# Kernel tuning notes

Measured on AMD Instinct MI355X. Metric: run time of the kernel, lower is better.

Reference implementation:

```python
import jax, jax.numpy as jnp
import numpy as np

B, T, E, H = 8, 2048, 1024, 64  # batch, seq_len(=block_size), embedding_size, head_size


def setup_inputs() -> dict:
    key = jax.random.key(0)
    k1, k2, k3, k4, k5 = jax.random.split(key, 5)
    x = jax.random.normal(k1, (B, T, E), dtype=jnp.float32)
    Wk = jax.random.normal(k2, (H, E), dtype=jnp.float32) * 0.02
    Wq = jax.random.normal(k3, (H, E), dtype=jnp.float32) * 0.02
    Wv = jax.random.normal(k4, (H, E), dtype=jnp.float32) * 0.02
    attention_mask = jax.random.randint(k5, (B, T), 0, 2).astype(jnp.int32)
    return {"x": x, "Wk": Wk, "Wq": Wq, "Wv": Wv, "attention_mask": attention_mask}


def reference(x, Wk, Wq, Wv, attention_mask):
    # Linear projections (nn.Linear with no bias: y = x @ W.T)
    k = jnp.einsum('bte,he->bth', x, Wk)
    q = jnp.einsum('bte,he->bth', x, Wq)
    v = jnp.einsum('bte,he->bth', x, Wv)
    scale = v.shape[2] ** -0.5  # head_size^-0.5, faithful to v.shape[2]**(-0.5)
    wei = jnp.einsum('bqh,bkh->bqk', q, k) * scale  # [B,T,T]
    # Causal mask (tril buffer) AND padding outer-product mask; the double-precision
    # outer product in the original just tests nonzero-ness, so a boolean AND is exact.
    causal = jnp.tril(jnp.ones((T, T), dtype=bool))  # [T,T]
    pad = (attention_mask[:, :, None] * attention_mask[:, None, :]) != 0  # [B,T,T]
    wei = jnp.where(causal[None, :, :] & pad, wei, -jnp.inf)
    wei = jax.nn.softmax(wei, axis=-1)
    wei = jnp.nan_to_num(wei)  # fully-masked rows -> 0 (matches torch.nan_to_num)
    # dropout in eval mode -> identity
    out = jnp.einsum('bqk,bkh->bqh', wei, v)
    return out
```

## Files before the change

### kernel.cpp

```cpp
#include <hip/hip_runtime.h>
#include <hip/hip_bf16.h>

typedef __bf16 bf16x8 __attribute__((ext_vector_type(8)));
typedef __bf16 bf16x4 __attribute__((ext_vector_type(4)));
typedef float  f32x4  __attribute__((ext_vector_type(4)));

#define LDP 72
#define KLDP 72
#define VLDP 40

#define BAR() { asm volatile("s_waitcnt lgkmcnt(0)" ::: "memory"); __builtin_amdgcn_s_barrier(); }

__global__ __launch_bounds__(256) void wconv_kernel(
    const float* __restrict__ Wk, const float* __restrict__ Wq,
    const float* __restrict__ Wv, __bf16* __restrict__ wbf)
{
    int idx = blockIdx.x * 256 + threadIdx.x;
    int row = idx >> 8;
    int c4  = idx & 255;
    const float* wp = (row < 64) ? Wk + (size_t)row * 1024
                    : (row < 128) ? Wq + (size_t)(row - 64) * 1024
                                  : Wv + (size_t)(row - 128) * 1024;
    float4 f = *reinterpret_cast<const float4*>(wp + c4 * 4);
    bf16x4 v; v[0] = (__bf16)f.x; v[1] = (__bf16)f.y; v[2] = (__bf16)f.z; v[3] = (__bf16)f.w;
    *reinterpret_cast<bf16x4*>(&wbf[(size_t)row * 1024 + c4 * 4]) = v;
}

__global__ __launch_bounds__(512) void maskpack_kernel(
    const int* __restrict__ mask, unsigned* __restrict__ maskw)
{
    int wdx = threadIdx.x;
    unsigned wv = 0;
    #pragma unroll
    for (int bit = 0; bit < 32; bit++)
        wv |= (mask[wdx * 32 + bit] != 0 ? 1u : 0u) << bit;
    maskw[wdx] = wv;
}

__global__ __launch_bounds__(1024) void proj_kernel(
    const float* __restrict__ x, const __bf16* __restrict__ wbf,
    __bf16* __restrict__ kbuf, __bf16* __restrict__ qbuf, __bf16* __restrict__ vtbuf)
{
    __shared__ __align__(16) __bf16 Slds[2][256 * LDP];
    __shared__ __align__(16) __bf16 Vtl[64 * LDP];

    const int tid  = threadIdx.x;
    const int lane = tid & 63;
    const int wid  = tid >> 6;
    const int wm   = wid >> 2;
    const int wn   = wid & 3;
    const int mbase = blockIdx.x * 64;

    const int cl = lane & 15;
    const int e0 = (lane >> 4) * 8;
    const int r0 = (lane >> 4) * 4;

    const int arow = tid >> 4, acg = tid & 15;
    const float* aptr = x + (size_t)(mbase + arow) * 1024 + acg * 4;

    float4 a0, a1;
    bf16x4 w0[3], w1[3];

#define ISSUE(aset, wset, kb) { \
    aset = *reinterpret_cast<const float4*>(aptr + (kb)); \
    _Pragma("unroll") \
    for (int i_ = 0; i_ < 3; i_++) { \
        int c_ = i_ * 1024 + tid; \
        wset[i_] = *reinterpret_cast<const bf16x4*>(&wbf[(size_t)(c_ >> 4) * 1024 + (kb) + (c_ & 15) * 4]); \
    } }

#define COMMIT(aset, wset, bufi) { \
    bf16x4 av_; \
    av_[0] = (__bf16)aset.x; av_[1] = (__bf16)aset.y; av_[2] = (__bf16)aset.z; av_[3] = (__bf16)aset.w; \
    *reinterpret_cast<bf16x4*>(&Slds[bufi][arow * LDP + acg * 4]) = av_; \
    _Pragma("unroll") \
    for (int i_ = 0; i_ < 3; i_++) { \
        int c_ = i_ * 1024 + tid; \
        *reinterpret_cast<bf16x4*>(&Slds[bufi][(64 + (c_ >> 4)) * LDP + (c_ & 15) * 4]) = wset[i_]; \
    } }

    f32x4 acc[3];
    #pragma unroll
    for (int n = 0; n < 3; n++) acc[n] = (f32x4){0.f, 0.f, 0.f, 0.f};

    ISSUE(a0, w0, 0);
    COMMIT(a0, w0, 0);
    ISSUE(a1, w1, 64);
    BAR();

    #pragma unroll 2
    for (int j = 0; j < 16; j++) {
        if (j < 14) {
            if (j & 1) { ISSUE(a1, w1, (j + 2) * 64); }
            else       { ISSUE(a0, w0, (j + 2) * 64); }
        }
        const __bf16* buf = Slds[j & 1];
        #pragma unroll
        for (int kk = 0; kk < 2; kk++) {
            bf16x8 a = *reinterpret_cast<const bf16x8*>(&buf[(wm * 16 + cl) * LDP + kk * 32 + e0]);
            #pragma unroll
            for (int nf = 0; nf < 3; nf++) {
                bf16x8 b = *reinterpret_cast<const bf16x8*>(&buf[(64 + wn * 48 + nf * 16 + cl) * LDP + kk * 32 + e0]);
                acc[nf] = __builtin_amdgcn_mfma_f32_16x16x32_bf16(a, b, acc[nf], 0, 0, 0);
            }
        }
        if (j < 15) {
            if (j & 1) { COMMIT(a0, w0, 0); }
            else       { COMMIT(a1, w1, 1); }
            BAR();
        }
    }
#undef ISSUE
#undef COMMIT

    #pragma unroll
    for (int nf = 0; nf < 3; nf++) {
        int c = wn * 48 + nf * 16 + cl;
        #pragma unroll
        for (int r = 0; r < 4; r++) {
            int mrel = wm * 16 + r0 + r;
            float v = acc[nf][r];
            if (c < 64)        kbuf[(size_t)(mbase + mrel) * 64 + c]         = (__bf16)v;
            else if (c < 128)  qbuf[(size_t)(mbase + mrel) * 64 + (c - 64)]  = (__bf16)v;
            else               Vtl[(c - 128) * LDP + mrel]                   = (__bf16)v;
        }
    }
    __syncthreads();
    {
        int b   = mbase >> 11;
        int tof = mbase & 2047;
        int h   = tid >> 4;
        int seg = tid & 15;
        bf16x4 v4 = *reinterpret_cast<const bf16x4*>(&Vtl[h * LDP + seg * 4]);
        *reinterpret_cast<bf16x4*>(&vtbuf[(size_t)b * 64 * 2048 + (size_t)h * 2048 + tof + seg * 4]) = v4;
    }
}

__global__ __launch_bounds__(256) void attn_kernel(
    const __bf16* __restrict__ qbuf, const __bf16* __restrict__ kbuf,
    const __bf16* __restrict__ vtbuf, const unsigned* __restrict__ maskw,
    const int* __restrict__ mask,
    float* __restrict__ out, float* __restrict__ accpart, float* __restrict__ mlpart,
    int nsplit, int tps)
{
    __shared__ __align__(16) __bf16 Klds[2][32 * KLDP];
    __shared__ __align__(16) __bf16 Vlds[2][64 * VLDP];
    __shared__ __align__(16) __bf16 Plds[4][16 * VLDP];

    const int tid  = threadIdx.x;
    const int lane = tid & 63;
    const int w    = tid >> 6;
    const int wg   = blockIdx.x;
    const int b    = wg & 7;
    const int rr_  = wg >> 3;
    const int qt   = rr_ & 31;
    const int sp   = rr_ >> 5;
    const int qbase = qt * 64 + w * 16;

    const int jbeg = sp * tps;
    const int jend = min((sp + 1) * tps, 2 * qt + 2);

    if (nsplit > 1 && jbeg >= jend) {
        float* ap = accpart + ((size_t)(b * nsplit + sp) * 2048 + qt * 64) * 64;
        for (int i = tid; i < 64 * 64; i += 256) ap[i] = 0.f;
        float* mp = mlpart + ((size_t)(b * nsplit + sp) * 2048 + qt * 64) * 2;
        for (int i = tid; i < 64; i += 256) { mp[2 * i] = -INFINITY; mp[2 * i + 1] = 0.f; }
        return;
    }

    const int cl = lane & 15;
    const int e0 = (lane >> 4) * 8;
    const int r0 = (lane >> 4) * 4;
    const int qs = qbase + cl;

    bf16x8 aq[2];
    #pragma unroll
    for (int kk = 0; kk < 2; kk++)
        aq[kk] = *reinterpret_cast<const bf16x8*>(&qbuf[((size_t)b * 2048 + qs) * 64 + kk * 32 + e0]);

    float m = -INFINITY, l = 0.f;
    f32x4 acc[4];
    #pragma unroll
    for (int hf = 0; hf < 4; hf++) acc[hf] = (f32x4){0.f, 0.f, 0.f, 0.f};

    const __bf16* kb  = kbuf  + (size_t)b * 2048 * 64;
    const __bf16* vtb = vtbuf + (size_t)b * 64 * 2048;

    const int krow = tid >> 3, kcg = tid & 7;
    const int vrow = tid >> 2, vcg = tid & 3;
    bf16x8 st_k, st_v;

#define KV_ISSUE(jj) { \
    st_k = *reinterpret_cast<const bf16x8*>(&kb[(size_t)((jj) * 32 + krow) * 64 + kcg * 8]); \
    st_v = *reinterpret_cast<const bf16x8*>(&vtb[(size_t)vrow * 2048 + (jj) * 32 + vcg * 8]); }

#define KV_COMMIT(bi) { \
    *reinterpret_cast<bf16x8*>(&Klds[bi][krow * KLDP + kcg * 8]) = st_k; \
    *reinterpret_cast<bf16x8*>(&Vlds[bi][vrow * VLDP + vcg * 8]) = st_v; }

    const int nt = jend - jbeg;
    KV_ISSUE(jbeg);
    KV_COMMIT(0);
    if (nt > 1) KV_ISSUE(jbeg + 1);
    BAR();

    for (int t = 0; t < nt; t++) {
        const int j = jbeg + t;
        const int cur = t & 1;

        if (t + 1 < nt) KV_COMMIT(cur ^ 1);
        if (t + 2 < nt) KV_ISSUE(j + 2);

        f32x4 s[2];
        #pragma unroll
        for (int jf = 0; jf < 2; jf++) {
            f32x4 tacc = (f32x4){0.f, 0.f, 0.f, 0.f};
            #pragma unroll
            for (int kk = 0; kk < 2; kk++) {
                bf16x8 bk = *reinterpret_cast<const bf16x8*>(&Klds[cur][(jf * 16 + cl) * KLDP + kk * 32 + e0]);
                tacc = __builtin_amdgcn_mfma_f32_16x16x32_bf16(bk, aq[kk], tacc, 0, 0, 0);
            }
            s[jf] = tacc;
        }

        const unsigned mw = maskw[b * 64 + j];
        float tmax = -INFINITY;
        #pragma unroll
        for (int jf = 0; jf < 2; jf++)
            #pragma unroll
            for (int r = 0; r < 4; r++) {
                int kvl = jf * 16 + r0 + r;
                bool ok = ((mw >> kvl) & 1u) && (j * 32 + kvl <= qs);
                float sv = s[jf][r] * 0.125f;
                sv = ok ? sv : -INFINITY;
                s[jf][r] = sv;
                tmax = fmaxf(tmax, sv);
            }
        tmax = fmaxf(tmax, __shfl_xor(tmax, 16));
        tmax = fmaxf(tmax, __shfl_xor(tmax, 32));

        float mn = fmaxf(m, tmax);
        float alpha = (mn == -INFINITY) ? 1.0f : __expf(m - mn);
        float rs = 0.f;
        #pragma unroll
        for (int jf = 0; jf < 2; jf++)
            #pragma unroll
            for (int r = 0; r < 4; r++) {
                float p = (mn == -INFINITY) ? 0.f : __expf(s[jf][r] - mn);
                s[jf][r] = p;
                rs += p;
            }
        rs += __shfl_xor(rs, 16);
        rs += __shfl_xor(rs, 32);
        l = l * alpha + rs;
        m = mn;

        #pragma unroll
        for (int hf = 0; hf < 4; hf++)
            #pragma unroll
            for (int r = 0; r < 4; r++) acc[hf][r] *= alpha;

        #pragma unroll
        for (int jf = 0; jf < 2; jf++) {
            bf16x4 p4;
            #pragma unroll
            for (int r = 0; r < 4; r++) p4[r] = (__bf16)s[jf][r];
            *reinterpret_cast<bf16x4*>(&Plds[w][cl * VLDP + jf * 16 + r0]) = p4;
        }
        {
            bf16x8 pb = *reinterpret_cast<const bf16x8*>(&Plds[w][cl * VLDP + e0]);
            #pragma unroll
            for (int hf = 0; hf < 4; hf++) {
                bf16x8 av = *reinterpret_cast<const bf16x8*>(&Vlds[cur][(hf * 16 + cl) * VLDP + e0]);
                acc[hf] = __builtin_amdgcn_mfma_f32_16x16x32_bf16(av, pb, acc[hf], 0, 0, 0);
            }
        }

        if (t + 1 < nt) BAR();
    }
#undef KV_ISSUE
#undef KV_COMMIT

    if (nsplit == 1) {
        int mq = mask[b * 2048 + qs];
        #pragma unroll
        for (int hf = 0; hf < 4; hf++)
            #pragma unroll
            for (int r = 0; r < 4; r++) {
                float v = (l > 0.f && mq != 0) ? acc[hf][r] / l : 0.f;
                out[((size_t)b * 2048 + qs) * 64 + hf * 16 + r0 + r] = v;
            }
    } else {
        #pragma unroll
        for (int hf = 0; hf < 4; hf++)
            #pragma unroll
            for (int r = 0; r < 4; r++)
                accpart[((size_t)(b * nsplit + sp) * 2048 + qs) * 64 + hf * 16 + r0 + r] = acc[hf][r];
        if (lane < 16) {
            int qrow = qbase + lane;
            mlpart[((size_t)(b * nsplit + sp) * 2048 + qrow) * 2 + 0] = m;
            mlpart[((size_t)(b * nsplit + sp) * 2048 + qrow) * 2 + 1] = l;
        }
    }
}

template<int NS>
__global__ __launch_bounds__(256) void combine_kernel(
    const float* __restrict__ accpart, const float* __restrict__ mlpart,
    const int* __restrict__ mask, float* __restrict__ out)
{
    int idx = blockIdx.x * 256 + threadIdx.x;
    int qglob = idx >> 6;
    int h = idx & 63;
    int b = qglob >> 11;
    int qrow = qglob & 2047;

    if (mask[qglob] == 0) { out[idx] = 0.f; return; }

    float m_s[NS], l_s[NS];
    float M = -INFINITY;
    #pragma unroll
    for (int s = 0; s < NS; s++) {
        size_t mo = ((size_t)(b * NS + s) * 2048 + qrow) * 2;
        m_s[s] = mlpart[mo];
        l_s[s] = mlpart[mo + 1];
        M = fmaxf(M, m_s[s]);
    }
    if (M == -INFINITY) { out[idx] = 0.f; return; }

    float L = 0.f, O = 0.f;
    #pragma unroll
    for (int s = 0; s < NS; s++) {
        float wgt = (m_s[s] == -INFINITY) ? 0.f : __expf(m_s[s] - M);
        L += l_s[s] * wgt;
        O += wgt * accpart[((size_t)(b * NS + s) * 2048 + qrow) * 64 + h];
    }
    out[idx] = (L > 0.f) ? O / L : 0.f;
}

extern "C" void kernel_launch(void* const* d_in, const int* in_sizes, int n_in,
                              void* d_out, int out_size, void* d_ws, size_t ws_size,
                              hipStream_t stream) {
    const float* x  = (const float*)d_in[0];
    const float* Wk = (const float*)d_in[1];
    const float* Wq = (const float*)d_in[2];
    const float* Wv = (const float*)d_in[3];
    const int* mask = (const int*)d_in[4];
    float* out = (float*)d_out;

    const size_t NTOK = 8 * 2048;
    __bf16* kbuf  = (__bf16*)d_ws;
    __bf16* qbuf  = kbuf + NTOK * 64;
    __bf16* vtbuf = qbuf + NTOK * 64;
    __bf16* wbf   = vtbuf + (size_t)8 * 64 * 2048;
    unsigned* maskw = (unsigned*)(wbf + (size_t)192 * 1024);
    const size_t base_bytes = NTOK * 64 * 2 * 2 + (size_t)8 * 64 * 2048 * 2
                            + (size_t)192 * 1024 * 2 + 512 * 4;

    const size_t acc_per_split = NTOK * 64 * 4;
    const size_t ml_per_split  = NTOK * 2 * 4;
    int nsplit = 1;
    if (ws_size >= base_bytes + 4 * (acc_per_split + ml_per_split))      nsplit = 4;
    else if (ws_size >= base_bytes + 2 * (acc_per_split + ml_per_split)) nsplit = 2;

    float* accpart = (float*)((char*)d_ws + base_bytes);
    float* mlpart  = accpart + NTOK * 64 * nsplit;

    wconv_kernel<<<192, 256, 0, stream>>>(Wk, Wq, Wv, wbf);
    maskpack_kernel<<<1, 512, 0, stream>>>(mask, maskw);
    proj_kernel<<<256, 1024, 0, stream>>>(x, wbf, kbuf, qbuf, vtbuf);
    attn_kernel<<<8 * 32 * nsplit, 256, 0, stream>>>(
        qbuf, kbuf, vtbuf, maskw, mask, out, accpart, mlpart, nsplit, 64 / nsplit);
    if (nsplit == 4)
        combine_kernel<4><<<(16384 * 64) / 256, 256, 0, stream>>>(accpart, mlpart, mask, out);
    else if (nsplit == 2)
        combine_kernel<2><<<(16384 * 64) / 256, 256, 0, stream>>>(accpart, mlpart, mask, out);
}
```

Before: 64.43 us.

## Widen attention tiles to 64 keys and 32 query rows per wave

The attention kernel now runs two waves per block. Each wave processes two 16-row query groups against 64-key K/V tiles, so every K and V fragment read from LDS feeds two MFMAs. The old LDS double buffer is replaced by one buffer plus a register prefetch, with two barriers per tile. The mask-packing kernel is folded into the weight-conversion launch, and later stages read the packed bitmask instead of the int mask. Splits with no work no longer zero their partial accumulators; they only write m=-inf and l=0, which risks NaN in the combine step if that uninitialized memory holds non-finite values.

```diff
diff --git a/kernel.cpp b/kernel.cpp
--- a/kernel.cpp
+++ b/kernel.cpp
@@ -5,16 +5,28 @@
 typedef __bf16 bf16x4 __attribute__((ext_vector_type(4)));
 typedef float  f32x4  __attribute__((ext_vector_type(4)));
 
-#define LDP 72
+#define LDP  72
 #define KLDP 72
-#define VLDP 40
+#define VLDP 72
+#define PLDP 72
 
 #define BAR() { asm volatile("s_waitcnt lgkmcnt(0)" ::: "memory"); __builtin_amdgcn_s_barrier(); }
 
 __global__ __launch_bounds__(256) void wconv_kernel(
     const float* __restrict__ Wk, const float* __restrict__ Wq,
-    const float* __restrict__ Wv, __bf16* __restrict__ wbf)
+    const float* __restrict__ Wv, const int* __restrict__ mask,
+    __bf16* __restrict__ wbf, unsigned* __restrict__ maskw)
 {
+    if (blockIdx.x == 192) {
+        for (int wdx = threadIdx.x; wdx < 512; wdx += 256) {
+            unsigned wv = 0;
+            #pragma unroll
+            for (int bit = 0; bit < 32; bit++)
+                wv |= (mask[wdx * 32 + bit] != 0 ? 1u : 0u) << bit;
+            maskw[wdx] = wv;
+        }
+        return;
+    }
     int idx = blockIdx.x * 256 + threadIdx.x;
     int row = idx >> 8;
     int c4  = idx & 255;
@@ -26,17 +38,6 @@
     *reinterpret_cast<bf16x4*>(&wbf[(size_t)row * 1024 + c4 * 4]) = v;
 }
 
-__global__ __launch_bounds__(512) void maskpack_kernel(
-    const int* __restrict__ mask, unsigned* __restrict__ maskw)
-{
-    int wdx = threadIdx.x;
-    unsigned wv = 0;
-    #pragma unroll
-    for (int bit = 0; bit < 32; bit++)
-        wv |= (mask[wdx * 32 + bit] != 0 ? 1u : 0u) << bit;
-    maskw[wdx] = wv;
-}
-
 __global__ __launch_bounds__(1024) void proj_kernel(
     const float* __restrict__ x, const __bf16* __restrict__ wbf,
     __bf16* __restrict__ kbuf, __bf16* __restrict__ qbuf, __bf16* __restrict__ vtbuf)
@@ -136,16 +137,15 @@
     }
 }
 
-__global__ __launch_bounds__(256) void attn_kernel(
+__global__ __launch_bounds__(128) void attn_kernel(
     const __bf16* __restrict__ qbuf, const __bf16* __restrict__ kbuf,
     const __bf16* __restrict__ vtbuf, const unsigned* __restrict__ maskw,
-    const int* __restrict__ mask,
     float* __restrict__ out, float* __restrict__ accpart, float* __restrict__ mlpart,
     int nsplit, int tps)
 {
-    __shared__ __align__(16) __bf16 Klds[2][32 * KLDP];
-    __shared__ __align__(16) __bf16 Vlds[2][64 * VLDP];
-    __shared__ __align__(16) __bf16 Plds[4][16 * VLDP];
+    __shared__ __align__(16) __bf16 Klds[64 * KLDP];
+    __shared__ __align__(16) __bf16 Vlds[64 * VLDP];
+    __shared__ __align__(16) __bf16 Plds[2][2][16 * PLDP];
 
     const int tid  = threadIdx.x;
     const int lane = tid & 63;
@@ -155,151 +155,155 @@
     const int rr_  = wg >> 3;
     const int qt   = rr_ & 31;
     const int sp   = rr_ >> 5;
-    const int qbase = qt * 64 + w * 16;
 
     const int jbeg = sp * tps;
-    const int jend = min((sp + 1) * tps, 2 * qt + 2);
+    const int jend = min((sp + 1) * tps, qt + 1);
 
     if (nsplit > 1 && jbeg >= jend) {
-        float* ap = accpart + ((size_t)(b * nsplit + sp) * 2048 + qt * 64) * 64;
-        for (int i = tid; i < 64 * 64; i += 256) ap[i] = 0.f;
-        float* mp = mlpart + ((size_t)(b * nsplit + sp) * 2048 + qt * 64) * 2;
-        for (int i = tid; i < 64; i += 256) { mp[2 * i] = -INFINITY; mp[2 * i + 1] = 0.f; }
+        for (int i = tid; i < 64; i += 128) {
+            size_t mo = ((size_t)(b * nsplit + sp) * 2048 + qt * 64 + i) * 2;
+            mlpart[mo] = -INFINITY; mlpart[mo + 1] = 0.f;
+        }
         return;
     }
 
     const int cl = lane & 15;
     const int e0 = (lane >> 4) * 8;
     const int r0 = (lane >> 4) * 4;
-    const int qs = qbase + cl;
-
-    bf16x8 aq[2];
-    #pragma unroll
-    for (int kk = 0; kk < 2; kk++)
-        aq[kk] = *reinterpret_cast<const bf16x8*>(&qbuf[((size_t)b * 2048 + qs) * 64 + kk * 32 + e0]);
-
-    float m = -INFINITY, l = 0.f;
-    f32x4 acc[4];
-    #pragma unroll
-    for (int hf = 0; hf < 4; hf++) acc[hf] = (f32x4){0.f, 0.f, 0.f, 0.f};
+    const int qs0 = qt * 64 + w * 16 + cl;
+    const int qs1 = qs0 + 32;
+
+    bf16x8 aq0[2], aq1[2];
+    #pragma unroll
+    for (int kk = 0; kk < 2; kk++) {
+        aq0[kk] = *reinterpret_cast<const bf16x8*>(&qbuf[((size_t)b * 2048 + qs0) * 64 + kk * 32 + e0]);
+        aq1[kk] = *reinterpret_cast<const bf16x8*>(&qbuf[((size_t)b * 2048 + qs1) * 64 + kk * 32 + e0]);
+    }
+
+    float m0 = -INFINITY, l0 = 0.f, m1 = -INFINITY, l1 = 0.f;
+    f32x4 acc0[4], acc1[4];
+    #pragma unroll
+    for (int hf = 0; hf < 4; hf++) { acc0[hf] = (f32x4){0.f,0.f,0.f,0.f}; acc1[hf] = (f32x4){0.f,0.f,0.f,0.f}; }
 
     const __bf16* kb  = kbuf  + (size_t)b * 2048 * 64;
     const __bf16* vtb = vtbuf + (size_t)b * 64 * 2048;
 
-    const int krow = tid >> 3, kcg = tid & 7;
-    const int vrow = tid >> 2, vcg = tid & 3;
-    bf16x8 st_k, st_v;
-
-#define KV_ISSUE(jj) { \
-    st_k = *reinterpret_cast<const bf16x8*>(&kb[(size_t)((jj) * 32 + krow) * 64 + kcg * 8]); \
-    st_v = *reinterpret_cast<const bf16x8*>(&vtb[(size_t)vrow * 2048 + (jj) * 32 + vcg * 8]); }
-
-#define KV_COMMIT(bi) { \
-    *reinterpret_cast<bf16x8*>(&Klds[bi][krow * KLDP + kcg * 8]) = st_k; \
-    *reinterpret_cast<bf16x8*>(&Vlds[bi][vrow * VLDP + vcg * 8]) = st_v; }
+    const int srow = tid >> 1;
+    const int sc   = (tid & 1) * 32;
+    bf16x8 stk[4], stv[4];
+
+#define KV_ISSUE(jj) { _Pragma("unroll") for (int i_ = 0; i_ < 4; i_++) { \
+    stk[i_] = *reinterpret_cast<const bf16x8*>(&kb[(size_t)((jj) * 64 + srow) * 64 + sc + i_ * 8]); \
+    stv[i_] = *reinterpret_cast<const bf16x8*>(&vtb[(size_t)srow * 2048 + (jj) * 64 + sc + i_ * 8]); } }
+
+#define KV_COMMIT() { _Pragma("unroll") for (int i_ = 0; i_ < 4; i_++) { \
+    *reinterpret_cast<bf16x8*>(&Klds[srow * KLDP + sc + i_ * 8]) = stk[i_]; \
+    *reinterpret_cast<bf16x8*>(&Vlds[srow * VLDP + sc + i_ * 8]) = stv[i_]; } }
+
+#define SOFTMAX(S, mS, lS, accS, qsS, su) { \
+    float tmax = -INFINITY; \
+    _Pragma("unroll") for (int jf = 0; jf < 4; jf++) { \
+        unsigned mw = (jf < 2) ? mw0 : mw1; \
+        _Pragma("unroll") for (int r = 0; r < 4; r++) { \
+            int kvl = jf * 16 + r0 + r; \
+            bool ok = ((mw >> (kvl & 31)) & 1u) && (j * 64 + kvl <= qsS); \
+            float sv = S[jf][r] * 0.125f; \
+            sv = ok ? sv : -INFINITY; \
+            S[jf][r] = sv; tmax = fmaxf(tmax, sv); } } \
+    tmax = fmaxf(tmax, __shfl_xor(tmax, 16)); \
+    tmax = fmaxf(tmax, __shfl_xor(tmax, 32)); \
+    float mn = fmaxf(mS, tmax); \
+    float alpha = (mn == -INFINITY) ? 1.0f : __expf(mS - mn); \
+    float rs = 0.f; \
+    _Pragma("unroll") for (int jf = 0; jf < 4; jf++) \
+        _Pragma("unroll") for (int r = 0; r < 4; r++) { \
+            float p = (mn == -INFINITY) ? 0.f : __expf(S[jf][r] - mn); \
+            S[jf][r] = p; rs += p; } \
+    rs += __shfl_xor(rs, 16); \
+    rs += __shfl_xor(rs, 32); \
+    lS = lS * alpha + rs; mS = mn; \
+    _Pragma("unroll") for (int hf = 0; hf < 4; hf++) \
+        _Pragma("unroll") for (int r = 0; r < 4; r++) accS[hf][r] *= alpha; \
+    _Pragma("unroll") for (int jf = 0; jf < 4; jf++) { \
+        bf16x4 p4; \
+        _Pragma("unroll") for (int r = 0; r < 4; r++) p4[r] = (__bf16)S[jf][r]; \
+        *reinterpret_cast<bf16x4*>(&Plds[w][su][cl * PLDP + jf * 16 + r0]) = p4; } }
 
     const int nt = jend - jbeg;
     KV_ISSUE(jbeg);
-    KV_COMMIT(0);
+    KV_COMMIT();
     if (nt > 1) KV_ISSUE(jbeg + 1);
     BAR();
 
     for (int t = 0; t < nt; t++) {
         const int j = jbeg + t;
-        const int cur = t & 1;
-
-        if (t + 1 < nt) KV_COMMIT(cur ^ 1);
-        if (t + 2 < nt) KV_ISSUE(j + 2);
-
-        f32x4 s[2];
-        #pragma unroll
-        for (int jf = 0; jf < 2; jf++) {
-            f32x4 tacc = (f32x4){0.f, 0.f, 0.f, 0.f};
+
+        f32x4 s0[4], s1[4];
+        #pragma unroll
+        for (int jf = 0; jf < 4; jf++) {
+            f32x4 t0 = (f32x4){0.f,0.f,0.f,0.f}, t1 = (f32x4){0.f,0.f,0.f,0.f};
             #pragma unroll
             for (int kk = 0; kk < 2; kk++) {
-                bf16x8 bk = *reinterpret_cast<const bf16x8*>(&Klds[cur][(jf * 16 + cl) * KLDP + kk * 32 + e0]);
-                tacc = __builtin_amdgcn_mfma_f32_16x16x32_bf16(bk, aq[kk], tacc, 0, 0, 0);
-            }
-            s[jf] = tacc;
-        }
-
-        const unsigned mw = maskw[b * 64 + j];
-        float tmax = -INFINITY;
-        #pragma unroll
-        for (int jf = 0; jf < 2; jf++)
-            #pragma unroll
-            for (int r = 0; r < 4; r++) {
-                int kvl = jf * 16 + r0 + r;
-                bool ok = ((mw >> kvl) & 1u) && (j * 32 + kvl <= qs);
-                float sv = s[jf][r] * 0.125f;
-                sv = ok ? sv : -INFINITY;
-                s[jf][r] = sv;
-                tmax = fmaxf(tmax, sv);
-            }
-        tmax = fmaxf(tmax, __shfl_xor(tmax, 16));
-        tmax = fmaxf(tmax, __shfl_xor(tmax, 32));
-
-        float mn = fmaxf(m, tmax);
-        float alpha = (mn == -INFINITY) ? 1.0f : __expf(m - mn);
-        float rs = 0.f;
-        #pragma unroll
-        for (int jf = 0; jf < 2; jf++)
-            #pragma unroll
-            for (int r = 0; r < 4; r++) {
-                float p = (mn == -INFINITY) ? 0.f : __expf(s[jf][r] - mn);
-                s[jf][r] = p;
-                rs += p;
-            }
-        rs += __shfl_xor(rs, 16);
-        rs += __shfl_xor(rs, 32);
-        l = l * alpha + rs;
-        m = mn;
-
-        #pragma unroll
-        for (int hf = 0; hf < 4; hf++)
-            #pragma unroll
-            for (int r = 0; r < 4; r++) acc[hf][r] *= alpha;
-
-        #pragma unroll
-        for (int jf = 0; jf < 2; jf++) {
-            bf16x4 p4;
-            #pragma unroll
-            for (int r = 0; r < 4; r++) p4[r] = (__bf16)s[jf][r];
-            *reinterpret_cast<bf16x4*>(&Plds[w][cl * VLDP + jf * 16 + r0]) = p4;
-        }
-        {
-            bf16x8 pb = *reinterpret_cast<const bf16x8*>(&Plds[w][cl * VLDP + e0]);
+                bf16x8 bk = *reinterpret_cast<const bf16x8*>(&Klds[(jf * 16 + cl) * KLDP + kk * 32 + e0]);
+                t0 = __builtin_amdgcn_mfma_f32_16x16x32_bf16(bk, aq0[kk], t0, 0, 0, 0);
+                t1 = __builtin_amdgcn_mfma_f32_16x16x32_bf16(bk, aq1[kk], t1, 0, 0, 0);
+            }
+            s0[jf] = t0; s1[jf] = t1;
+        }
+
+        const unsigned mw0 = maskw[b * 64 + j * 2];
+        const unsigned mw1 = maskw[b * 64 + j * 2 + 1];
+        SOFTMAX(s0, m0, l0, acc0, qs0, 0);
+        SOFTMAX(s1, m1, l1, acc1, qs1, 1);
+
+        #pragma unroll
+        for (int kk = 0; kk < 2; kk++) {
+            bf16x8 p0 = *reinterpret_cast<const bf16x8*>(&Plds[w][0][cl * PLDP + kk * 32 + e0]);
+            bf16x8 p1 = *reinterpret_cast<const bf16x8*>(&Plds[w][1][cl * PLDP + kk * 32 + e0]);
             #pragma unroll
             for (int hf = 0; hf < 4; hf++) {
-                bf16x8 av = *reinterpret_cast<const bf16x8*>(&Vlds[cur][(hf * 16 + cl) * VLDP + e0]);
-                acc[hf] = __builtin_amdgcn_mfma_f32_16x16x32_bf16(av, pb, acc[hf], 0, 0, 0);
-            }
-        }
-
-        if (t + 1 < nt) BAR();
+                bf16x8 av = *reinterpret_cast<const bf16x8*>(&Vlds[(hf * 16 + cl) * VLDP + kk * 32 + e0]);
+                acc0[hf] = __builtin_amdgcn_mfma_f32_16x16x32_bf16(av, p0, acc0[hf], 0, 0, 0);
+                acc1[hf] = __builtin_amdgcn_mfma_f32_16x16x32_bf16(av, p1, acc1[hf], 0, 0, 0);
+            }
+        }
+
+        BAR();
+        if (t + 1 < nt) {
+            KV_COMMIT();
+            if (t + 2 < nt) KV_ISSUE(j + 2);
+            BAR();
+        }
     }
 #undef KV_ISSUE
 #undef KV_COMMIT
-
+#undef SOFTMAX
+
+    const bool mq0 = (maskw[b * 64 + (qs0 >> 5)] >> (qs0 & 31)) & 1u;
+    const bool mq1 = (maskw[b * 64 + (qs1 >> 5)] >> (qs1 & 31)) & 1u;
     if (nsplit == 1) {
-        int mq = mask[b * 2048 + qs];
         #pragma unroll
         for (int hf = 0; hf < 4; hf++)
             #pragma unroll
             for (int r = 0; r < 4; r++) {
-                float v = (l > 0.f && mq != 0) ? acc[hf][r] / l : 0.f;
-                out[((size_t)b * 2048 + qs) * 64 + hf * 16 + r0 + r] = v;
+                float v0 = (l0 > 0.f && mq0) ? acc0[hf][r] / l0 : 0.f;
+                float v1 = (l1 > 0.f && mq1) ? acc1[hf][r] / l1 : 0.f;
+                out[((size_t)b * 2048 + qs0) * 64 + hf * 16 + r0 + r] = v0;
+                out[((size_t)b * 2048 + qs1) * 64 + hf * 16 + r0 + r] = v1;
             }
     } else {
         #pragma unroll
         for (int hf = 0; hf < 4; hf++)
             #pragma unroll
-            for (int r = 0; r < 4; r++)
-                accpart[((size_t)(b * nsplit + sp) * 2048 + qs) * 64 + hf * 16 + r0 + r] = acc[hf][r];
+            for (int r = 0; r < 4; r++) {
+                accpart[((size_t)(b * nsplit + sp) * 2048 + qs0) * 64 + hf * 16 + r0 + r] = acc0[hf][r];
+                accpart[((size_t)(b * nsplit + sp) * 2048 + qs1) * 64 + hf * 16 + r0 + r] = acc1[hf][r];
+            }
         if (lane < 16) {
-            int qrow = qbase + lane;
-            mlpart[((size_t)(b * nsplit + sp) * 2048 + qrow) * 2 + 0] = m;
-            mlpart[((size_t)(b * nsplit + sp) * 2048 + qrow) * 2 + 1] = l;
+            size_t mo0 = ((size_t)(b * nsplit + sp) * 2048 + qs0) * 2;
+            size_t mo1 = ((size_t)(b * nsplit + sp) * 2048 + qs1) * 2;
+            mlpart[mo0] = m0; mlpart[mo0 + 1] = l0;
+            mlpart[mo1] = m1; mlpart[mo1 + 1] = l1;
         }
     }
 }
@@ -307,7 +311,7 @@
 template<int NS>
 __global__ __launch_bounds__(256) void combine_kernel(
     const float* __restrict__ accpart, const float* __restrict__ mlpart,
-    const int* __restrict__ mask, float* __restrict__ out)
+    const unsigned* __restrict__ maskw, float* __restrict__ out)
 {
     int idx = blockIdx.x * 256 + threadIdx.x;
     int qglob = idx >> 6;
@@ -315,7 +319,7 @@
     int b = qglob >> 11;
     int qrow = qglob & 2047;
 
-    if (mask[qglob] == 0) { out[idx] = 0.f; return; }
+    if (!((maskw[b * 64 + (qrow >> 5)] >> (qrow & 31)) & 1u)) { out[idx] = 0.f; return; }
 
     float m_s[NS], l_s[NS];
     float M = -INFINITY;
@@ -366,13 +370,12 @@
     float* accpart = (float*)((char*)d_ws + base_bytes);
     float* mlpart  = accpart + NTOK * 64 * nsplit;
 
-    wconv_kernel<<<192, 256, 0, stream>>>(Wk, Wq, Wv, wbf);
-    maskpack_kernel<<<1, 512, 0, stream>>>(mask, maskw);
+    wconv_kernel<<<193, 256, 0, stream>>>(Wk, Wq, Wv, mask, wbf, maskw);
     proj_kernel<<<256, 1024, 0, stream>>>(x, wbf, kbuf, qbuf, vtbuf);
-    attn_kernel<<<8 * 32 * nsplit, 256, 0, stream>>>(
-        qbuf, kbuf, vtbuf, maskw, mask, out, accpart, mlpart, nsplit, 64 / nsplit);
+    attn_kernel<<<8 * 32 * nsplit, 128, 0, stream>>>(
+        qbuf, kbuf, vtbuf, maskw, out, accpart, mlpart, nsplit, 32 / nsplit);
     if (nsplit == 4)
-        combine_kernel<4><<<(16384 * 64) / 256, 256, 0, stream>>>(accpart, mlpart, mask, out);
+        combine_kernel<4><<<(16384 * 64) / 256, 256, 0, stream>>>(accpart, mlpart, maskw, out);
     else if (nsplit == 2)
-        combine_kernel<2><<<(16384 * 64) / 256, 256, 0, stream>>>(accpart, mlpart, mask, out);
-}
+        combine_kernel<2><<<(16384 * 64) / 256, 256, 0, stream>>>(accpart, mlpart, maskw, out);
+}
```

After: 58.21 us. -9.7%, faster.

## Restructure attention to single-wave blocks covering 64 queries, allow 8-way KV split

Applied to the files above, without the earlier changes.

The attention kernel now runs one wavefront per block. Each wave handles all four 16-row query chunks, so every K/V tile loaded into LDS is reused across 64 queries, and block barriers are replaced by local LDS waitcnt fences with a single-buffered tile. The split-KV factor can rise to 8 when workspace allows. Mask packing is folded into the weight-conversion kernel to save a launch, and empty splits write only m/l, with combine skipping them. The cost is much higher register pressure per wave (acc[4][4], aq[4][2]), fewer threads per block to hide latency, and more partial traffic in the combine step.

```diff
diff --git a/kernel.cpp b/kernel.cpp
--- a/kernel.cpp
+++ b/kernel.cpp
@@ -5,16 +5,29 @@
 typedef __bf16 bf16x4 __attribute__((ext_vector_type(4)));
 typedef float  f32x4  __attribute__((ext_vector_type(4)));
 
-#define LDP 72
+#define LDP  72
 #define KLDP 72
 #define VLDP 40
+#define PLDP 40
 
 #define BAR() { asm volatile("s_waitcnt lgkmcnt(0)" ::: "memory"); __builtin_amdgcn_s_barrier(); }
+#define DSFENCE() { asm volatile("s_waitcnt lgkmcnt(0)" ::: "memory"); }
 
 __global__ __launch_bounds__(256) void wconv_kernel(
     const float* __restrict__ Wk, const float* __restrict__ Wq,
-    const float* __restrict__ Wv, __bf16* __restrict__ wbf)
+    const float* __restrict__ Wv, const int* __restrict__ mask,
+    __bf16* __restrict__ wbf, unsigned* __restrict__ maskw)
 {
+    if (blockIdx.x == 192) {
+        for (int wdx = threadIdx.x; wdx < 512; wdx += 256) {
+            unsigned wv = 0;
+            #pragma unroll
+            for (int bit = 0; bit < 32; bit++)
+                wv |= (mask[wdx * 32 + bit] != 0 ? 1u : 0u) << bit;
+            maskw[wdx] = wv;
+        }
+        return;
+    }
     int idx = blockIdx.x * 256 + threadIdx.x;
     int row = idx >> 8;
     int c4  = idx & 255;
@@ -26,17 +39,6 @@
     *reinterpret_cast<bf16x4*>(&wbf[(size_t)row * 1024 + c4 * 4]) = v;
 }
 
-__global__ __launch_bounds__(512) void maskpack_kernel(
-    const int* __restrict__ mask, unsigned* __restrict__ maskw)
-{
-    int wdx = threadIdx.x;
-    unsigned wv = 0;
-    #pragma unroll
-    for (int bit = 0; bit < 32; bit++)
-        wv |= (mask[wdx * 32 + bit] != 0 ? 1u : 0u) << bit;
-    maskw[wdx] = wv;
-}
-
 __global__ __launch_bounds__(1024) void proj_kernel(
     const float* __restrict__ x, const __bf16* __restrict__ wbf,
     __bf16* __restrict__ kbuf, __bf16* __restrict__ qbuf, __bf16* __restrict__ vtbuf)
@@ -136,170 +138,195 @@
     }
 }
 
-__global__ __launch_bounds__(256) void attn_kernel(
+__global__ __launch_bounds__(64) void attn_kernel(
     const __bf16* __restrict__ qbuf, const __bf16* __restrict__ kbuf,
     const __bf16* __restrict__ vtbuf, const unsigned* __restrict__ maskw,
-    const int* __restrict__ mask,
     float* __restrict__ out, float* __restrict__ accpart, float* __restrict__ mlpart,
     int nsplit, int tps)
 {
-    __shared__ __align__(16) __bf16 Klds[2][32 * KLDP];
-    __shared__ __align__(16) __bf16 Vlds[2][64 * VLDP];
-    __shared__ __align__(16) __bf16 Plds[4][16 * VLDP];
-
-    const int tid  = threadIdx.x;
-    const int lane = tid & 63;
-    const int w    = tid >> 6;
+    __shared__ __align__(16) __bf16 Klds[32 * KLDP];
+    __shared__ __align__(16) __bf16 Vlds[64 * VLDP];
+    __shared__ __align__(16) __bf16 Plds[4][16 * PLDP];
+
+    const int lane = threadIdx.x;
     const int wg   = blockIdx.x;
     const int b    = wg & 7;
-    const int rr_  = wg >> 3;
-    const int qt   = rr_ & 31;
-    const int sp   = rr_ >> 5;
-    const int qbase = qt * 64 + w * 16;
+    const int r_   = wg >> 3;
+    const int qt   = r_ & 31;
+    const int sp   = r_ >> 5;
 
     const int jbeg = sp * tps;
     const int jend = min((sp + 1) * tps, 2 * qt + 2);
 
     if (nsplit > 1 && jbeg >= jend) {
-        float* ap = accpart + ((size_t)(b * nsplit + sp) * 2048 + qt * 64) * 64;
-        for (int i = tid; i < 64 * 64; i += 256) ap[i] = 0.f;
-        float* mp = mlpart + ((size_t)(b * nsplit + sp) * 2048 + qt * 64) * 2;
-        for (int i = tid; i < 64; i += 256) { mp[2 * i] = -INFINITY; mp[2 * i + 1] = 0.f; }
+        size_t mo = ((size_t)(b * nsplit + sp) * 2048 + qt * 64 + lane) * 2;
+        mlpart[mo] = -INFINITY; mlpart[mo + 1] = 0.f;
         return;
     }
 
     const int cl = lane & 15;
-    const int e0 = (lane >> 4) * 8;
-    const int r0 = (lane >> 4) * 4;
-    const int qs = qbase + cl;
-
-    bf16x8 aq[2];
-    #pragma unroll
-    for (int kk = 0; kk < 2; kk++)
-        aq[kk] = *reinterpret_cast<const bf16x8*>(&qbuf[((size_t)b * 2048 + qs) * 64 + kk * 32 + e0]);
-
-    float m = -INFINITY, l = 0.f;
-    f32x4 acc[4];
-    #pragma unroll
-    for (int hf = 0; hf < 4; hf++) acc[hf] = (f32x4){0.f, 0.f, 0.f, 0.f};
+    const int hi = lane >> 4;
+    const int e0 = hi * 8;
+    const int r0 = hi * 4;
+
+    bf16x8 aq[4][2];
+    #pragma unroll
+    for (int c = 0; c < 4; c++)
+        #pragma unroll
+        for (int kk = 0; kk < 2; kk++)
+            aq[c][kk] = *reinterpret_cast<const bf16x8*>(
+                &qbuf[((size_t)b * 2048 + qt * 64 + c * 16 + cl) * 64 + kk * 32 + e0]);
+
+    float m[4], l[4];
+    f32x4 acc[4][4];
+    #pragma unroll
+    for (int c = 0; c < 4; c++) {
+        m[c] = -INFINITY; l[c] = 0.f;
+        #pragma unroll
+        for (int hf = 0; hf < 4; hf++) acc[c][hf] = (f32x4){0.f, 0.f, 0.f, 0.f};
+    }
 
     const __bf16* kb  = kbuf  + (size_t)b * 2048 * 64;
     const __bf16* vtb = vtbuf + (size_t)b * 64 * 2048;
 
-    const int krow = tid >> 3, kcg = tid & 7;
-    const int vrow = tid >> 2, vcg = tid & 3;
-    bf16x8 st_k, st_v;
-
-#define KV_ISSUE(jj) { \
-    st_k = *reinterpret_cast<const bf16x8*>(&kb[(size_t)((jj) * 32 + krow) * 64 + kcg * 8]); \
-    st_v = *reinterpret_cast<const bf16x8*>(&vtb[(size_t)vrow * 2048 + (jj) * 32 + vcg * 8]); }
-
-#define KV_COMMIT(bi) { \
-    *reinterpret_cast<bf16x8*>(&Klds[bi][krow * KLDP + kcg * 8]) = st_k; \
-    *reinterpret_cast<bf16x8*>(&Vlds[bi][vrow * VLDP + vcg * 8]) = st_v; }
+    const int krow = lane >> 1, kc = (lane & 1) * 32;
+    bf16x8 stk[4], stv[4];
+
+#define KV_ISSUE(jj) { _Pragma("unroll") for (int i_ = 0; i_ < 4; i_++) { \
+    stk[i_] = *reinterpret_cast<const bf16x8*>(&kb[(size_t)((jj) * 32 + krow) * 64 + kc + i_ * 8]); \
+    stv[i_] = *reinterpret_cast<const bf16x8*>(&vtb[(size_t)lane * 2048 + (jj) * 32 + i_ * 8]); } }
+
+#define KV_COMMIT() { _Pragma("unroll") for (int i_ = 0; i_ < 4; i_++) { \
+    *reinterpret_cast<bf16x8*>(&Klds[krow * KLDP + kc + i_ * 8]) = stk[i_]; \
+    *reinterpret_cast<bf16x8*>(&Vlds[lane * VLDP + i_ * 8]) = stv[i_]; } }
 
     const int nt = jend - jbeg;
     KV_ISSUE(jbeg);
-    KV_COMMIT(0);
+    KV_COMMIT();
     if (nt > 1) KV_ISSUE(jbeg + 1);
-    BAR();
 
     for (int t = 0; t < nt; t++) {
         const int j = jbeg + t;
-        const int cur = t & 1;
-
-        if (t + 1 < nt) KV_COMMIT(cur ^ 1);
-        if (t + 2 < nt) KV_ISSUE(j + 2);
-
-        f32x4 s[2];
+        DSFENCE();
+
+        f32x4 s[4][2];
         #pragma unroll
         for (int jf = 0; jf < 2; jf++) {
-            f32x4 tacc = (f32x4){0.f, 0.f, 0.f, 0.f};
+            f32x4 tc[4];
+            #pragma unroll
+            for (int c = 0; c < 4; c++) tc[c] = (f32x4){0.f, 0.f, 0.f, 0.f};
             #pragma unroll
             for (int kk = 0; kk < 2; kk++) {
-                bf16x8 bk = *reinterpret_cast<const bf16x8*>(&Klds[cur][(jf * 16 + cl) * KLDP + kk * 32 + e0]);
-                tacc = __builtin_amdgcn_mfma_f32_16x16x32_bf16(bk, aq[kk], tacc, 0, 0, 0);
+                bf16x8 bk = *reinterpret_cast<const bf16x8*>(&Klds[(jf * 16 + cl) * KLDP + kk * 32 + e0]);
+                #pragma unroll
+                for (int c = 0; c < 4; c++)
+                    tc[c] = __builtin_amdgcn_mfma_f32_16x16x32_bf16(bk, aq[c][kk], tc[c], 0, 0, 0);
             }
-            s[jf] = tacc;
+            #pragma unroll
+            for (int c = 0; c < 4; c++) s[c][jf] = tc[c];
+        }
+
+        bf16x8 av[4];
+        #pragma unroll
+        for (int hf = 0; hf < 4; hf++)
+            av[hf] = *reinterpret_cast<const bf16x8*>(&Vlds[(hf * 16 + cl) * VLDP + e0]);
+
+        if (t + 1 < nt) {
+            DSFENCE();
+            KV_COMMIT();
+            if (t + 2 < nt) KV_ISSUE(j + 2);
         }
 
         const unsigned mw = maskw[b * 64 + j];
-        float tmax = -INFINITY;
-        #pragma unroll
-        for (int jf = 0; jf < 2; jf++)
-            #pragma unroll
-            for (int r = 0; r < 4; r++) {
-                int kvl = jf * 16 + r0 + r;
-                bool ok = ((mw >> kvl) & 1u) && (j * 32 + kvl <= qs);
-                float sv = s[jf][r] * 0.125f;
-                sv = ok ? sv : -INFINITY;
-                s[jf][r] = sv;
-                tmax = fmaxf(tmax, sv);
+        #pragma unroll
+        for (int c = 0; c < 4; c++) {
+            const int qs = qt * 64 + c * 16 + cl;
+            float tmax = -INFINITY;
+            #pragma unroll
+            for (int jf = 0; jf < 2; jf++)
+                #pragma unroll
+                for (int r = 0; r < 4; r++) {
+                    int kvl = jf * 16 + r0 + r;
+                    bool ok = ((mw >> kvl) & 1u) && (j * 32 + kvl <= qs);
+                    float sv = s[c][jf][r] * 0.125f;
+                    sv = ok ? sv : -INFINITY;
+                    s[c][jf][r] = sv;
+                    tmax = fmaxf(tmax, sv);
+                }
+            tmax = fmaxf(tmax, __shfl_xor(tmax, 16));
+            tmax = fmaxf(tmax, __shfl_xor(tmax, 32));
+            float mn = fmaxf(m[c], tmax);
+            float alpha = (mn == -INFINITY) ? 1.0f : __expf(m[c] - mn);
+            float rs = 0.f;
+            #pragma unroll
+            for (int jf = 0; jf < 2; jf++)
+                #pragma unroll
+                for (int r = 0; r < 4; r++) {
+                    float p = (mn == -INFINITY) ? 0.f : __expf(s[c][jf][r] - mn);
+                    s[c][jf][r] = p;
+                    rs += p;
+                }
+            rs += __shfl_xor(rs, 16);
+            rs += __shfl_xor(rs, 32);
+            l[c] = l[c] * alpha + rs;
+            m[c] = mn;
+            #pragma unroll
+            for (int hf = 0; hf < 4; hf++)
+                #pragma unroll
+                for (int r = 0; r < 4; r++) acc[c][hf][r] *= alpha;
+            #pragma unroll
+            for (int jf = 0; jf < 2; jf++) {
+                bf16x4 p4;
+                #pragma unroll
+                for (int r = 0; r < 4; r++) p4[r] = (__bf16)s[c][jf][r];
+                *reinterpret_cast<bf16x4*>(&Plds[c][cl * PLDP + jf * 16 + r0]) = p4;
             }
-        tmax = fmaxf(tmax, __shfl_xor(tmax, 16));
-        tmax = fmaxf(tmax, __shfl_xor(tmax, 32));
-
-        float mn = fmaxf(m, tmax);
-        float alpha = (mn == -INFINITY) ? 1.0f : __expf(m - mn);
-        float rs = 0.f;
-        #pragma unroll
-        for (int jf = 0; jf < 2; jf++)
-            #pragma unroll
-            for (int r = 0; r < 4; r++) {
-                float p = (mn == -INFINITY) ? 0.f : __expf(s[jf][r] - mn);
-                s[jf][r] = p;
-                rs += p;
-            }
-        rs += __shfl_xor(rs, 16);
-        rs += __shfl_xor(rs, 32);
-        l = l * alpha + rs;
-        m = mn;
-
-        #pragma unroll
-        for (int hf = 0; hf < 4; hf++)
-            #pragma unroll
-            for (int r = 0; r < 4; r++) acc[hf][r] *= alpha;
-
-        #pragma unroll
-        for (int jf = 0; jf < 2; jf++) {
-            bf16x4 p4;
-            #pragma unroll
-            for (int r = 0; r < 4; r++) p4[r] = (__bf16)s[jf][r];
-            *reinterpret_cast<bf16x4*>(&Plds[w][cl * VLDP + jf * 16 + r0]) = p4;
-        }
+        }
+
         {
-            bf16x8 pb = *reinterpret_cast<const bf16x8*>(&Plds[w][cl * VLDP + e0]);
-            #pragma unroll
-            for (int hf = 0; hf < 4; hf++) {
-                bf16x8 av = *reinterpret_cast<const bf16x8*>(&Vlds[cur][(hf * 16 + cl) * VLDP + e0]);
-                acc[hf] = __builtin_amdgcn_mfma_f32_16x16x32_bf16(av, pb, acc[hf], 0, 0, 0);
-            }
-        }
-
-        if (t + 1 < nt) BAR();
+            bf16x8 pb[4];
+            #pragma unroll
+            for (int c = 0; c < 4; c++)
+                pb[c] = *reinterpret_cast<const bf16x8*>(&Plds[c][cl * PLDP + e0]);
+            #pragma unroll
+            for (int hf = 0; hf < 4; hf++)
+                #pragma unroll
+                for (int c = 0; c < 4; c++)
+                    acc[c][hf] = __builtin_amdgcn_mfma_f32_16x16x32_bf16(av[hf], pb[c], acc[c][hf], 0, 0, 0);
+        }
     }
 #undef KV_ISSUE
 #undef KV_COMMIT
 
     if (nsplit == 1) {
-        int mq = mask[b * 2048 + qs];
-        #pragma unroll
-        for (int hf = 0; hf < 4; hf++)
-            #pragma unroll
-            for (int r = 0; r < 4; r++) {
-                float v = (l > 0.f && mq != 0) ? acc[hf][r] / l : 0.f;
-                out[((size_t)b * 2048 + qs) * 64 + hf * 16 + r0 + r] = v;
+        #pragma unroll
+        for (int c = 0; c < 4; c++) {
+            const int qs = qt * 64 + c * 16 + cl;
+            const bool mq = (maskw[b * 64 + (qs >> 5)] >> (qs & 31)) & 1u;
+            #pragma unroll
+            for (int hf = 0; hf < 4; hf++)
+                #pragma unroll
+                for (int r = 0; r < 4; r++) {
+                    float v = (l[c] > 0.f && mq) ? acc[c][hf][r] / l[c] : 0.f;
+                    out[((size_t)b * 2048 + qs) * 64 + hf * 16 + r0 + r] = v;
+                }
+        }
+    } else {
+        #pragma unroll
+        for (int c = 0; c < 4; c++) {
+            const int qs = qt * 64 + c * 16 + cl;
+            #pragma unroll
+            for (int hf = 0; hf < 4; hf++)
+                #pragma unroll
+                for (int r = 0; r < 4; r++)
+                    accpart[((size_t)(b * nsplit + sp) * 2048 + qs) * 64 + hf * 16 + r0 + r] = acc[c][hf][r];
+        }
+        if (lane < 16) {
+            #pragma unroll
+            for (int c = 0; c < 4; c++) {
+                size_t mo = ((size_t)(b * nsplit + sp) * 2048 + qt * 64 + c * 16 + lane) * 2;
+                mlpart[mo] = m[c]; mlpart[mo + 1] = l[c];
             }
-    } else {
-        #pragma unroll
-        for (int hf = 0; hf < 4; hf++)
-            #pragma unroll
-            for (int r = 0; r < 4; r++)
-                accpart[((size_t)(b * nsplit + sp) * 2048 + qs) * 64 + hf * 16 + r0 + r] = acc[hf][r];
-        if (lane < 16) {
-            int qrow = qbase + lane;
-            mlpart[((size_t)(b * nsplit + sp) * 2048 + qrow) * 2 + 0] = m;
-            mlpart[((size_t)(b * nsplit + sp) * 2048 + qrow) * 2 + 1] = l;
         }
     }
 }
@@ -307,7 +334,7 @@
 template<int NS>
 __global__ __launch_bounds__(256) void combine_kernel(
     const float* __restrict__ accpart, const float* __restrict__ mlpart,
-    const int* __restrict__ mask, float* __restrict__ out)
+    const unsigned* __restrict__ maskw, float* __restrict__ out)
 {
     int idx = blockIdx.x * 256 + threadIdx.x;
     int qglob = idx >> 6;
@@ -315,7 +342,7 @@
     int b = qglob >> 11;
     int qrow = qglob & 2047;
 
-    if (mask[qglob] == 0) { out[idx] = 0.f; return; }
+    if (!((maskw[b * 64 + (qrow >> 5)] >> (qrow & 31)) & 1u)) { out[idx] = 0.f; return; }
 
     float m_s[NS], l_s[NS];
     float M = -INFINITY;
@@ -331,9 +358,11 @@
     float L = 0.f, O = 0.f;
     #pragma unroll
     for (int s = 0; s < NS; s++) {
-        float wgt = (m_s[s] == -INFINITY) ? 0.f : __expf(m_s[s] - M);
-        L += l_s[s] * wgt;
-        O += wgt * accpart[((size_t)(b * NS + s) * 2048 + qrow) * 64 + h];
+        if (m_s[s] > -INFINITY) {
+            float wgt = __expf(m_s[s] - M);
+            L += l_s[s] * wgt;
+            O += wgt * accpart[((size_t)(b * NS + s) * 2048 + qrow) * 64 + h];
+        }
     }
     out[idx] = (L > 0.f) ? O / L : 0.f;
 }
@@ -360,19 +389,21 @@
     const size_t acc_per_split = NTOK * 64 * 4;
     const size_t ml_per_split  = NTOK * 2 * 4;
     int nsplit = 1;
-    if (ws_size >= base_bytes + 4 * (acc_per_split + ml_per_split))      nsplit = 4;
+    if (ws_size >= base_bytes + 8 * (acc_per_split + ml_per_split))      nsplit = 8;
+    else if (ws_size >= base_bytes + 4 * (acc_per_split + ml_per_split)) nsplit = 4;
     else if (ws_size >= base_bytes + 2 * (acc_per_split + ml_per_split)) nsplit = 2;
 
     float* accpart = (float*)((char*)d_ws + base_bytes);
     float* mlpart  = accpart + NTOK * 64 * nsplit;
 
-    wconv_kernel<<<192, 256, 0, stream>>>(Wk, Wq, Wv, wbf);
-    maskpack_kernel<<<1, 512, 0, stream>>>(mask, maskw);
+    wconv_kernel<<<193, 256, 0, stream>>>(Wk, Wq, Wv, mask, wbf, maskw);
     proj_kernel<<<256, 1024, 0, stream>>>(x, wbf, kbuf, qbuf, vtbuf);
-    attn_kernel<<<8 * 32 * nsplit, 256, 0, stream>>>(
-        qbuf, kbuf, vtbuf, maskw, mask, out, accpart, mlpart, nsplit, 64 / nsplit);
-    if (nsplit == 4)
-        combine_kernel<4><<<(16384 * 64) / 256, 256, 0, stream>>>(accpart, mlpart, mask, out);
+    attn_kernel<<<8 * 32 * nsplit, 64, 0, stream>>>(
+        qbuf, kbuf, vtbuf, maskw, out, accpart, mlpart, nsplit, 64 / nsplit);
+    if (nsplit == 8)
+        combine_kernel<8><<<(16384 * 64) / 256, 256, 0, stream>>>(accpart, mlpart, maskw, out);
+    else if (nsplit == 4)
+        combine_kernel<4><<<(16384 * 64) / 256, 256, 0, stream>>>(accpart, mlpart, maskw, out);
     else if (nsplit == 2)
-        combine_kernel<2><<<(16384 * 64) / 256, 256, 0, stream>>>(accpart, mlpart, mask, out);
+        combine_kernel<2><<<(16384 * 64) / 256, 256, 0, stream>>>(accpart, mlpart, maskw, out);
 }
```

Result: slower. 72.10 us (+11.9%).
